# Kernel tuning notes

Measured on AMD Instinct MI355X. Metric: run time of the kernel, lower is better.

## Reference

```python
import jax, jax.numpy as jnp
import numpy as np

B, NX, W, DX, DY, D, H, P = 8, 512, 16, 1536, 1024, 768, 12, 8


def setup_inputs() -> dict:
    key = jax.random.key(0)
    ks = jax.random.split(key, 12)
    r = lambda k, s: jax.random.normal(k, s, dtype=jnp.float32) * 0.02
    return {
        "x": jax.random.normal(ks[0], (B, NX, DX), jnp.float32),
        "y": jax.random.normal(ks[1], (B, NX * W, DY), jnp.float32),
        "Wx": r(ks[2], (DX, D)), "bx": jnp.zeros((D,), jnp.float32),
        "Wy": r(ks[3], (DY, D)), "by": jnp.zeros((D,), jnp.float32),
        "prompt": r(ks[4], (1, P, D)),
        "Wq": r(ks[5], (D, D)), "bq": jnp.zeros((D,), jnp.float32),
        "Wk": r(ks[6], (D, D)), "bk": jnp.zeros((D,), jnp.float32),
        "Wv": r(ks[7], (D, D)), "bv": jnp.zeros((D,), jnp.float32),
        "Wo": r(ks[8], (D, D)), "bo": jnp.zeros((D,), jnp.float32),
        "ln_g": jnp.ones((D,), jnp.float32), "ln_b": jnp.zeros((D,), jnp.float32),
    }


def _l2n(f, eps=1e-6):
    return f / (jnp.linalg.norm(f, axis=-1, keepdims=True) + eps)


def reference(x, y, Wx, bx, Wy, by, prompt, Wq, bq, Wk, bk, Wv, bv, Wo, bo, ln_g, ln_b):
    dh = D // H
    scale = 1.0 / jnp.sqrt(jnp.float32(dh))
    xp = _l2n(x @ Wx + bx)            # [B,NX,D]
    yp = _l2n(y @ Wy + by)            # [B,NX*W,D]
    # In the original, only normalized_output[:,0:1] is kept per window, and
    # per-query attention is independent, so only query index 0 contributes.
    q = ((xp[:, 0] @ Wq) + bq).reshape(B, H, dh) * scale   # [B,H,dh]
    yw = yp.reshape(B, NX, W, D)                            # 16-token windows
    k = ((yw @ Wk) + bk).reshape(B, NX, W, H, dh)
    v = ((yw @ Wv) + bv).reshape(B, NX, W, H, dh)
    s = jnp.einsum('bhd,bnwhd->bhnw', q, k)                # [B,H,NX,W]
    a = jax.nn.softmax(s, axis=-1)
    ctx = jnp.einsum('bhnw,bnwhd->bnhd', a, v).reshape(B, NX, D)
    o = ctx @ Wo + bo                                      # attn out_proj
    mu = jnp.mean(o, axis=-1, keepdims=True)
    var = jnp.var(o, axis=-1, keepdims=True)
    normed = (o - mu) / jnp.sqrt(var + 1e-6) * ln_g + ln_b  # [B,NX,D]
    blocks = jnp.concatenate(
        [normed[:, :, None, :],
         jnp.broadcast_to(prompt[:, None], (B, NX, P, D))], axis=2)  # [B,NX,1+P,D]
    return blocks.reshape(B, NX * (1 + P), D)
```

## Files before the change

kernel.cpp:

```cpp
#include <hip/hip_runtime.h>
#include <stdint.h>

#define BQ 8
#define NXQ 512
#define WQ 16
#define DXQ 1536
#define DYQ 1024
#define DQ 768
#define HQ 12
#define PQ 8
#define MY 65536
#define BN_ROWS 4096

typedef __attribute__((ext_vector_type(8))) short short8;
typedef __attribute__((ext_vector_type(4))) float f32x4;
typedef unsigned short ushort_t;
typedef unsigned int uint_t;

__device__ __forceinline__ ushort_t f2bf(float f) {
  uint_t u = __float_as_uint(f);
  u += 0x7FFFu + ((u >> 16) & 1u);
  return (ushort_t)(u >> 16);
}
__device__ __forceinline__ float bf2f(ushort_t h) {
  return __uint_as_float(((uint_t)h) << 16);
}
__device__ __forceinline__ void gload_lds16(const void* g, void* l) {
  __builtin_amdgcn_global_load_lds(
      (__attribute__((address_space(1))) unsigned int*)(g),
      (__attribute__((address_space(3))) unsigned int*)(l), 16, 0, 0);
}

__global__ void k_conv(const float* __restrict__ y, const float* __restrict__ Wy,
                       const float* __restrict__ Wv, const float* __restrict__ Wo,
                       ushort_t* __restrict__ ybf, ushort_t* __restrict__ WyT,
                       ushort_t* __restrict__ WvT, ushort_t* __restrict__ WoT,
                       float* __restrict__ rowsq, float* __restrict__ oS12,
                       float* __restrict__ xw) {
  const int gstride = gridDim.x * blockDim.x;
  const int g0 = blockIdx.x * blockDim.x + threadIdx.x;
  const int NY8 = MY * DYQ / 8;
  for (int i = g0; i < NY8; i += gstride) {
    const float4* s = (const float4*)(y + (size_t)i * 8);
    float4 f0 = s[0], f1 = s[1];
    short8 hv;
    hv[0] = (short)f2bf(f0.x); hv[1] = (short)f2bf(f0.y);
    hv[2] = (short)f2bf(f0.z); hv[3] = (short)f2bf(f0.w);
    hv[4] = (short)f2bf(f1.x); hv[5] = (short)f2bf(f1.y);
    hv[6] = (short)f2bf(f1.z); hv[7] = (short)f2bf(f1.w);
    *(short8*)(ybf + (size_t)i * 8) = hv;
  }
  for (int i = g0; i < MY; i += gstride) rowsq[i] = 0.f;
  for (int i = g0; i < 2 * BN_ROWS; i += gstride) oS12[i] = 0.f;
  for (int i = g0; i < BQ * DQ; i += gstride) xw[i] = 0.f;
  const int N1 = DQ * DYQ;
  const int N2 = DQ * DQ;
  const int total = N1 + 2 * N2;
  for (int i = g0; i < total; i += gstride) {
    if (i < N1) {
      int n = i / DYQ, k = i - n * DYQ;
      WyT[i] = f2bf(Wy[k * DQ + n]);
    } else if (i < N1 + N2) {
      int j = i - N1;
      int n = j / DQ, k = j - n * DQ;
      WvT[j] = f2bf(Wv[k * DQ + n]);
    } else {
      int j = i - N1 - N2;
      int n = j / DQ, k = j - n * DQ;
      WoT[j] = f2bf(Wo[k * DQ + n]);
    }
  }
}

__global__ __launch_bounds__(128) void k_q1(const float* __restrict__ x,
                                            const float* __restrict__ Wx,
                                            const float* __restrict__ bx,
                                            float* __restrict__ xw) {
  const int b = blockIdx.x, c = blockIdx.y * 128 + threadIdx.x;
  const int kc = blockIdx.z;
  const float* xr = x + (size_t)b * NXQ * DXQ + kc * 192;
  const float* wp = Wx + (size_t)kc * 192 * DQ + c;
  float acc = (kc == 0) ? bx[c] : 0.f;
  for (int k = 0; k < 192; ++k) acc += xr[k] * wp[(size_t)k * DQ];
  atomicAdd(&xw[b * DQ + c], acc);
}

__global__ __launch_bounds__(128) void k_q2(const float* __restrict__ xw,
                                            const float* __restrict__ Wq,
                                            const float* __restrict__ bq,
                                            float* __restrict__ qv) {
  const int b = blockIdx.x, c = blockIdx.y * 128 + threadIdx.x;
  const float* xr = xw + b * DQ;
  float acc = 0.f, ss = 0.f;
  for (int k = 0; k < DQ; ++k) {
    float v = xr[k];
    acc += v * Wq[(size_t)k * DQ + c];
    ss += v * v;
  }
  const float inv = 1.0f / (sqrtf(ss) + 1e-6f);
  qv[b * DQ + c] = (acc * inv + bq[c]) * 0.125f;
}

__global__ void k_q3(const float* __restrict__ Wk, const float* __restrict__ bk,
                     const float* __restrict__ qv, float* __restrict__ qk,
                     float* __restrict__ cQ) {
  const int bh = blockIdx.x;
  const int b = bh / HQ, h = bh - b * HQ;
  const int tid = threadIdx.x;
  const float* q = qv + b * DQ + h * 64;
#pragma unroll
  for (int j = 0; j < 3; ++j) {
    int dd = tid + j * 256;
    float acc = 0.f;
    for (int j2 = 0; j2 < 64; ++j2) acc += Wk[(size_t)dd * DQ + h * 64 + j2] * q[j2];
    qk[(size_t)bh * DQ + dd] = acc;
  }
  if (tid == 0) {
    float acc = 0.f;
    for (int j2 = 0; j2 < 64; ++j2) acc += q[j2] * bk[h * 64 + j2];
    cQ[bh] = acc;
  }
}

#define YP_TSZ 49152
#define YP_NT 16
__global__ __launch_bounds__(512) void k_gemm_yp(const ushort_t* __restrict__ ybf,
                                                 const ushort_t* __restrict__ WyT,
                                                 const float* __restrict__ by,
                                                 ushort_t* __restrict__ z,
                                                 float* __restrict__ rowsqg) {
  __shared__ __align__(16) char smem[3 * YP_TSZ + 1024];
  float* rowsq_l = (float*)(smem + 3 * YP_TSZ);
  const int tid = threadIdx.x, lane = tid & 63, wv = tid >> 6;
  const int wvM = wv >> 2, wvN = wv & 3;
  const int g = blockIdx.x;
  const int m = (g / 48) * 8 + (g & 7);
  const int n = (g >> 3) % 6;
  const int mBase = m * 256, nBase = n * 128;
  if (tid < 256) rowsq_l[tid] = 0.f;

  const int l8 = lane >> 3;
  const int c8 = (lane & 7) ^ (l8 & 7);
  const ushort_t* aSrc[4]; const ushort_t* bSrc[2];
  int aDst[4], bDst[2];
#pragma unroll
  for (int j = 0; j < 4; ++j) {
    int r = wv * 32 + j * 8 + l8;
    aSrc[j] = ybf + (size_t)(mBase + r) * DYQ + c8 * 8;
    aDst[j] = (wv * 32 + j * 8) * 128;
  }
#pragma unroll
  for (int j = 0; j < 2; ++j) {
    int r = wv * 16 + j * 8 + l8;
    bSrc[j] = WyT + (size_t)(nBase + r) * DYQ + c8 * 8;
    bDst[j] = 32768 + (wv * 16 + j * 8) * 128;
  }
  const int q = lane >> 4;
  int aRowB[8], aSw[8], bRowB[2], bSw[2];
#pragma unroll
  for (int mf = 0; mf < 8; ++mf) {
    int r = wvM * 128 + mf * 16 + (lane & 15);
    aRowB[mf] = r * 128; aSw[mf] = r & 7;
  }
#pragma unroll
  for (int nf = 0; nf < 2; ++nf) {
    int r = wvN * 32 + nf * 16 + (lane & 15);
    bRowB[nf] = 32768 + r * 128; bSw[nf] = r & 7;
  }

#define YP_STAGE(dbuf, t)                                                      \
  {                                                                            \
    char* db = smem + (dbuf) * YP_TSZ;                                         \
    _Pragma("unroll") for (int j = 0; j < 4; ++j)                              \
        gload_lds16(aSrc[j] + (t) * 64, db + aDst[j]);                         \
    _Pragma("unroll") for (int j = 0; j < 2; ++j)                              \
        gload_lds16(bSrc[j] + (t) * 64, db + bDst[j]);                         \
  }

  f32x4 acc[8][2] = {};
  YP_STAGE(0, 0);
  YP_STAGE(1, 1);
  int bR = 0, bS = 2;
  for (int t = 0; t < YP_NT; ++t) {
    if (t < YP_NT - 1) {
      asm volatile("s_waitcnt vmcnt(6)" ::: "memory");
    } else {
      asm volatile("s_waitcnt vmcnt(0)" ::: "memory");
    }
    __builtin_amdgcn_s_barrier();
    __builtin_amdgcn_sched_barrier(0);
    if (t + 2 < YP_NT) YP_STAGE(bS, t + 2);
    const char* cur = smem + bR * YP_TSZ;
#pragma unroll
    for (int ks = 0; ks < 2; ++ks) {
      short8 af[8], bf[2];
#pragma unroll
      for (int mf = 0; mf < 8; ++mf)
        af[mf] = *(const short8*)(cur + aRowB[mf] + (((ks * 4 + q) ^ aSw[mf]) << 4));
#pragma unroll
      for (int nf = 0; nf < 2; ++nf)
        bf[nf] = *(const short8*)(cur + bRowB[nf] + (((ks * 4 + q) ^ bSw[nf]) << 4));
      __builtin_amdgcn_s_setprio(1);
#pragma unroll
      for (int nf = 0; nf < 2; ++nf)
#pragma unroll
        for (int mf = 0; mf < 8; ++mf)
          acc[mf][nf] = __builtin_amdgcn_mfma_f32_16x16x32_bf16(af[mf], bf[nf],
                                                                acc[mf][nf], 0, 0, 0);
      __builtin_amdgcn_s_setprio(0);
    }
    __builtin_amdgcn_sched_barrier(0);
    bR = (bR == 2) ? 0 : bR + 1;
    bS = (bS == 2) ? 0 : bS + 1;
  }
  __syncthreads();

  float byv[2];
#pragma unroll
  for (int nf = 0; nf < 2; ++nf) byv[nf] = by[nBase + wvN * 32 + nf * 16 + (lane & 15)];
#pragma unroll
  for (int mf = 0; mf < 8; ++mf) {
#pragma unroll
    for (int rr = 0; rr < 4; ++rr) {
      int row_l = wvM * 128 + mf * 16 + (lane >> 4) * 4 + rr;
      float ss = 0.f;
#pragma unroll
      for (int nf = 0; nf < 2; ++nf) {
        float zv = acc[mf][nf][rr] + byv[nf];
        ss += zv * zv;
        int col_l = wvN * 32 + nf * 16 + (lane & 15);
        *(ushort_t*)(smem + row_l * 256 + col_l * 2) = f2bf(zv);
      }
#pragma unroll
      for (int o = 1; o < 16; o <<= 1) ss += __shfl_xor(ss, o, 64);
      if ((lane & 15) == 0) atomicAdd(&rowsq_l[row_l], ss);
    }
  }
  __syncthreads();
  if (tid < 256) atomicAdd(&rowsqg[mBase + tid], rowsq_l[tid]);
#pragma unroll
  for (int it = 0; it < 8; ++it) {
    int row = it * 32 + (tid >> 4);
    int ch = tid & 15;
    uint4 v = *(const uint4*)(smem + row * 256 + ch * 16);
    *(uint4*)(z + (size_t)(mBase + row) * DQ + nBase + ch * 8) = v;
  }
}

__global__ __launch_bounds__(256) void k_attn(const ushort_t* __restrict__ z,
                                              const float* __restrict__ rowsqg,
                                              const float* __restrict__ qk,
                                              const float* __restrict__ cQ,
                                              ushort_t* __restrict__ p) {
  __shared__ __align__(16) char smem[16 * 1552 + 192 * 4 * 2 + 64];
  float* s_l = (float*)(smem + 16 * 1552);
  float* a_l = s_l + 192;
  float* inv_l = a_l + 192;
  const int bn = blockIdx.x, b = bn >> 9;
  const int tid = threadIdx.x;
  if (tid < 16) inv_l[tid] = 1.0f / (sqrtf(rowsqg[bn * 16 + tid]) + 1e-6f);
  for (int j = tid; j < 16 * 96; j += 256) {
    int w = j / 96, ch = j - w * 96;
    *(short8*)(smem + w * 1552 + ch * 16) =
        *(const short8*)(z + ((size_t)bn * 16 + w) * DQ + ch * 8);
  }
  __syncthreads();
  if (tid < 192) {
    int h = tid >> 4, w = tid & 15;
    const float4* qkp = (const float4*)(qk + (size_t)(b * HQ + h) * DQ);
    float acc = 0.f;
    const char* yrow = smem + w * 1552;
    for (int dc = 0; dc < 192; ++dc) {
      float4 q4 = qkp[dc];
      uint2 hh = *(const uint2*)(yrow + dc * 8);
      acc += q4.x * bf2f((ushort_t)(hh.x & 0xffff));
      acc += q4.y * bf2f((ushort_t)(hh.x >> 16));
      acc += q4.z * bf2f((ushort_t)(hh.y & 0xffff));
      acc += q4.w * bf2f((ushort_t)(hh.y >> 16));
    }
    s_l[tid] = acc * inv_l[w] + cQ[b * HQ + h];
  }
  __syncthreads();
  if (tid < 12) {
    float mx = -1e30f;
#pragma unroll
    for (int w = 0; w < 16; ++w) mx = fmaxf(mx, s_l[tid * 16 + w]);
    float sm = 0.f, ev[16];
#pragma unroll
    for (int w = 0; w < 16; ++w) {
      ev[w] = __expf(s_l[tid * 16 + w] - mx);
      sm += ev[w];
    }
    float rden = 1.0f / sm;
#pragma unroll
    for (int w = 0; w < 16; ++w) a_l[tid * 16 + w] = ev[w] * rden * inv_l[w];
  }
  __syncthreads();
  float zr[16][3];
#pragma unroll
  for (int w = 0; w < 16; ++w)
#pragma unroll
    for (int i = 0; i < 3; ++i)
      zr[w][i] = bf2f(*(const ushort_t*)(smem + w * 1552 + (tid + i * 256) * 2));
  for (int h = 0; h < HQ; ++h) {
    float acc0 = 0.f, acc1 = 0.f, acc2 = 0.f;
#pragma unroll
    for (int w = 0; w < 16; ++w) {
      float aw = a_l[h * 16 + w];
      acc0 += aw * zr[w][0];
      acc1 += aw * zr[w][1];
      acc2 += aw * zr[w][2];
    }
    size_t base = ((size_t)bn * HQ + h) * DQ + tid;
    p[base] = f2bf(acc0);
    p[base + 256] = f2bf(acc1);
    p[base + 512] = f2bf(acc2);
  }
}

#define PV_TSZ 24576
__global__ __launch_bounds__(256) void k_gemm_pv(const ushort_t* __restrict__ p,
                                                 const ushort_t* __restrict__ WvT,
                                                 const float* __restrict__ bv,
                                                 ushort_t* __restrict__ ctx) {
  __shared__ __align__(16) char smem[3 * PV_TSZ];
  const int tid = threadIdx.x, lane = tid & 63, wv = tid >> 6;
  const int wvM = wv >> 1, wvN = wv & 1;
  const int mBase = blockIdx.x * 128, h = blockIdx.y;
  const int l8 = lane >> 3;
  const int c8 = (lane & 7) ^ (l8 & 7);
  const ushort_t* aSrc[4]; const ushort_t* bSrc[2];
  int aDst[4], bDst[2];
#pragma unroll
  for (int j = 0; j < 4; ++j) {
    int r = wv * 32 + j * 8 + l8;
    aSrc[j] = p + ((size_t)(mBase + r) * HQ + h) * DQ + c8 * 8;
    aDst[j] = (wv * 32 + j * 8) * 128;
  }
#pragma unroll
  for (int j = 0; j < 2; ++j) {
    int r = wv * 16 + j * 8 + l8;
    bSrc[j] = WvT + (size_t)(h * 64 + r) * DQ + c8 * 8;
    bDst[j] = 16384 + (wv * 16 + j * 8) * 128;
  }
  const int q = lane >> 4;
  int aRowB[4], aSw[4], bRowB[2], bSw[2];
#pragma unroll
  for (int mf = 0; mf < 4; ++mf) {
    int r = wvM * 64 + mf * 16 + (lane & 15);
    aRowB[mf] = r * 128; aSw[mf] = r & 7;
  }
#pragma unroll
  for (int nf = 0; nf < 2; ++nf) {
    int r = wvN * 32 + nf * 16 + (lane & 15);
    bRowB[nf] = 16384 + r * 128; bSw[nf] = r & 7;
  }
#define PV_STAGE(dbuf, t)                                                      \
  {                                                                            \
    char* db = smem + (dbuf) * PV_TSZ;                                         \
    _Pragma("unroll") for (int j = 0; j < 4; ++j)                              \
        gload_lds16(aSrc[j] + (t) * 64, db + aDst[j]);                         \
    _Pragma("unroll") for (int j = 0; j < 2; ++j)                              \
        gload_lds16(bSrc[j] + (t) * 64, db + bDst[j]);                         \
  }
  f32x4 acc[4][2] = {};
  PV_STAGE(0, 0);
  PV_STAGE(1, 1);
  int bR = 0, bS = 2;
  for (int t = 0; t < 12; ++t) {
    if (t < 11) {
      asm volatile("s_waitcnt vmcnt(6)" ::: "memory");
    } else {
      asm volatile("s_waitcnt vmcnt(0)" ::: "memory");
    }
    __builtin_amdgcn_s_barrier();
    __builtin_amdgcn_sched_barrier(0);
    if (t + 2 < 12) PV_STAGE(bS, t + 2);
    const char* cur = smem + bR * PV_TSZ;
#pragma unroll
    for (int ks = 0; ks < 2; ++ks) {
      short8 af[4], bf[2];
#pragma unroll
      for (int mf = 0; mf < 4; ++mf)
        af[mf] = *(const short8*)(cur + aRowB[mf] + (((ks * 4 + q) ^ aSw[mf]) << 4));
#pragma unroll
      for (int nf = 0; nf < 2; ++nf)
        bf[nf] = *(const short8*)(cur + bRowB[nf] + (((ks * 4 + q) ^ bSw[nf]) << 4));
      __builtin_amdgcn_s_setprio(1);
#pragma unroll
      for (int nf = 0; nf < 2; ++nf)
#pragma unroll
        for (int mf = 0; mf < 4; ++mf)
          acc[mf][nf] = __builtin_amdgcn_mfma_f32_16x16x32_bf16(af[mf], bf[nf],
                                                                acc[mf][nf], 0, 0, 0);
      __builtin_amdgcn_s_setprio(0);
    }
    __builtin_amdgcn_sched_barrier(0);
    bR = (bR == 2) ? 0 : bR + 1;
    bS = (bS == 2) ? 0 : bS + 1;
  }
#pragma unroll
  for (int nf = 0; nf < 2; ++nf) {
    int col = h * 64 + wvN * 32 + nf * 16 + (lane & 15);
    float bvv = bv[col];
#pragma unroll
    for (int mf = 0; mf < 4; ++mf)
#pragma unroll
      for (int rr = 0; rr < 4; ++rr) {
        int row = mBase + wvM * 64 + mf * 16 + (lane >> 4) * 4 + rr;
        ctx[(size_t)row * DQ + col] = f2bf(acc[mf][nf][rr] + bvv);
      }
  }
}

__global__ __launch_bounds__(256) void k_gemm_o(const ushort_t* __restrict__ ctx,
                                                const ushort_t* __restrict__ WoT,
                                                const float* __restrict__ bo,
                                                float* __restrict__ o,
                                                float* __restrict__ oS12) {
  __shared__ __align__(16) char smem[3 * PV_TSZ];
  const int tid = threadIdx.x, lane = tid & 63, wv = tid >> 6;
  const int wvM = wv >> 1, wvN = wv & 1;
  const int mBase = blockIdx.x * 128, nBase = blockIdx.y * 64;
  const int l8 = lane >> 3;
  const int c8 = (lane & 7) ^ (l8 & 7);
  const ushort_t* aSrc[4]; const ushort_t* bSrc[2];
  int aDst[4], bDst[2];
#pragma unroll
  for (int j = 0; j < 4; ++j) {
    int r = wv * 32 + j * 8 + l8;
    aSrc[j] = ctx + (size_t)(mBase + r) * DQ + c8 * 8;
    aDst[j] = (wv * 32 + j * 8) * 128;
  }
#pragma unroll
  for (int j = 0; j < 2; ++j) {
    int r = wv * 16 + j * 8 + l8;
    bSrc[j] = WoT + (size_t)(nBase + r) * DQ + c8 * 8;
    bDst[j] = 16384 + (wv * 16 + j * 8) * 128;
  }
  const int q = lane >> 4;
  int aRowB[4], aSw[4], bRowB[2], bSw[2];
#pragma unroll
  for (int mf = 0; mf < 4; ++mf) {
    int r = wvM * 64 + mf * 16 + (lane & 15);
    aRowB[mf] = r * 128; aSw[mf] = r & 7;
  }
#pragma unroll
  for (int nf = 0; nf < 2; ++nf) {
    int r = wvN * 32 + nf * 16 + (lane & 15);
    bRowB[nf] = 16384 + r * 128; bSw[nf] = r & 7;
  }
  f32x4 acc[4][2] = {};
#define O_STAGE(dbuf, t)                                                       \
  {                                                                            \
    char* db = smem + (dbuf) * PV_TSZ;                                         \
    _Pragma("unroll") for (int j = 0; j < 4; ++j)                              \
        gload_lds16(aSrc[j] + (t) * 64, db + aDst[j]);                         \
    _Pragma("unroll") for (int j = 0; j < 2; ++j)                              \
        gload_lds16(bSrc[j] + (t) * 64, db + bDst[j]);                         \
  }
  O_STAGE(0, 0);
  O_STAGE(1, 1);
  int bR = 0, bS = 2;
  for (int t = 0; t < 12; ++t) {
    if (t < 11) {
      asm volatile("s_waitcnt vmcnt(6)" ::: "memory");
    } else {
      asm volatile("s_waitcnt vmcnt(0)" ::: "memory");
    }
    __builtin_amdgcn_s_barrier();
    __builtin_amdgcn_sched_barrier(0);
    if (t + 2 < 12) O_STAGE(bS, t + 2);
    const char* cur = smem + bR * PV_TSZ;
#pragma unroll
    for (int ks = 0; ks < 2; ++ks) {
      short8 af[4], bf[2];
#pragma unroll
      for (int mf = 0; mf < 4; ++mf)
        af[mf] = *(const short8*)(cur + aRowB[mf] + (((ks * 4 + q) ^ aSw[mf]) << 4));
#pragma unroll
      for (int nf = 0; nf < 2; ++nf)
        bf[nf] = *(const short8*)(cur + bRowB[nf] + (((ks * 4 + q) ^ bSw[nf]) << 4));
      __builtin_amdgcn_s_setprio(1);
#pragma unroll
      for (int nf = 0; nf < 2; ++nf)
#pragma unroll
        for (int mf = 0; mf < 4; ++mf)
          acc[mf][nf] = __builtin_amdgcn_mfma_f32_16x16x32_bf16(af[mf], bf[nf],
                                                                acc[mf][nf], 0, 0, 0);
      __builtin_amdgcn_s_setprio(0);
    }
    __builtin_amdgcn_sched_barrier(0);
    bR = (bR == 2) ? 0 : bR + 1;
    bS = (bS == 2) ? 0 : bS + 1;
  }
  float bo0 = bo[nBase + wvN * 32 + (lane & 15)];
  float bo1 = bo[nBase + wvN * 32 + 16 + (lane & 15)];
#pragma unroll
  for (int mf = 0; mf < 4; ++mf)
#pragma unroll
    for (int rr = 0; rr < 4; ++rr) {
      int row = mBase + wvM * 64 + mf * 16 + (lane >> 4) * 4 + rr;
      float z0 = acc[mf][0][rr] + bo0;
      float z1 = acc[mf][1][rr] + bo1;
      o[(size_t)row * DQ + nBase + wvN * 32 + (lane & 15)] = z0;
      o[(size_t)row * DQ + nBase + wvN * 32 + 16 + (lane & 15)] = z1;
      float s1 = z0 + z1, s2 = z0 * z0 + z1 * z1;
#pragma unroll
      for (int ofs = 1; ofs < 16; ofs <<= 1) {
        s1 += __shfl_xor(s1, ofs, 64);
        s2 += __shfl_xor(s2, ofs, 64);
      }
      if ((lane & 15) == 0) {
        atomicAdd(&oS12[row], s1);
        atomicAdd(&oS12[BN_ROWS + row], s2);
      }
    }
}

__global__ __launch_bounds__(256) void k_out(const float* __restrict__ o,
                                             const float* __restrict__ oS12,
                                             const float* __restrict__ ln_g,
                                             const float* __restrict__ ln_b,
                                             const float* __restrict__ prompt,
                                             float* __restrict__ out) {
  const int row = blockIdx.x;
  const int tid = threadIdx.x;
  float mu = oS12[row] * (1.0f / DQ);
  float va = oS12[BN_ROWS + row] * (1.0f / DQ) - mu * mu;
  float rstd = rsqrtf(va + 1e-6f);
  int b = row >> 9, n = row & 511;
  size_t obase = ((size_t)b * (NXQ * (PQ + 1)) + (size_t)n * (PQ + 1)) * DQ;
#pragma unroll
  for (int j = 0; j < 3; ++j) {
    int col = tid + j * 256;
    out[obase + col] = (o[(size_t)row * DQ + col] - mu) * rstd * ln_g[col] + ln_b[col];
  }
#pragma unroll
  for (int pi = 0; pi < PQ; ++pi)
#pragma unroll
    for (int j = 0; j < 3; ++j) {
      int col = tid + j * 256;
      out[obase + (size_t)(1 + pi) * DQ + col] = prompt[pi * DQ + col];
    }
}

extern "C" void kernel_launch(void* const* d_in, const int* in_sizes, int n_in,
                              void* d_out, int out_size, void* d_ws, size_t ws_size,
                              hipStream_t stream) {
  (void)in_sizes; (void)n_in; (void)out_size; (void)ws_size;
  const float* x    = (const float*)d_in[0];
  const float* y    = (const float*)d_in[1];
  const float* Wx   = (const float*)d_in[2];
  const float* bx   = (const float*)d_in[3];
  const float* Wy   = (const float*)d_in[4];
  const float* by   = (const float*)d_in[5];
  const float* prom = (const float*)d_in[6];
  const float* Wq   = (const float*)d_in[7];
  const float* bq   = (const float*)d_in[8];
  const float* Wk   = (const float*)d_in[9];
  const float* bk   = (const float*)d_in[10];
  const float* Wv   = (const float*)d_in[11];
  const float* bv   = (const float*)d_in[12];
  const float* Wo   = (const float*)d_in[13];
  const float* bo   = (const float*)d_in[14];
  const float* lng  = (const float*)d_in[15];
  const float* lnb  = (const float*)d_in[16];
  float* out = (float*)d_out;
  char* ws = (char*)d_ws;

  size_t oWyT = 0;
  size_t oWvT = oWyT + (size_t)DQ * DYQ * 2;
  size_t oWoT = oWvT + (size_t)DQ * DQ * 2;
  size_t oXw  = oWoT + (size_t)DQ * DQ * 2;
  size_t oQ   = oXw + (size_t)BQ * DQ * 4 + 256;
  size_t oQK  = oQ + (size_t)BQ * DQ * 4;
  size_t oC   = oQK + (size_t)BQ * HQ * DQ * 4;
  size_t oRq  = oC + 1024;
  size_t oS   = oRq + (size_t)MY * 4;
  size_t oYbf = oS + (size_t)2 * BN_ROWS * 4;
  size_t oZ   = oYbf + (size_t)MY * DYQ * 2;
  size_t oP   = oYbf;
  size_t oCtx = oYbf + (size_t)BN_ROWS * HQ * DQ * 2;
  size_t oO   = oZ;

  ushort_t* WyT = (ushort_t*)(ws + oWyT);
  ushort_t* WvT = (ushort_t*)(ws + oWvT);
  ushort_t* WoT = (ushort_t*)(ws + oWoT);
  float* xw  = (float*)(ws + oXw);
  float* qv  = (float*)(ws + oQ);
  float* qk  = (float*)(ws + oQK);
  float* cQ  = (float*)(ws + oC);
  float* rowsq = (float*)(ws + oRq);
  float* oS12  = (float*)(ws + oS);
  ushort_t* ybf  = (ushort_t*)(ws + oYbf);
  ushort_t* zbuf = (ushort_t*)(ws + oZ);
  ushort_t* p    = (ushort_t*)(ws + oP);
  ushort_t* ctx  = (ushort_t*)(ws + oCtx);
  float* obuf    = (float*)(ws + oO);

  k_conv<<<dim3(4096), dim3(256), 0, stream>>>(y, Wy, Wv, Wo, ybf, WyT, WvT, WoT,
                                               rowsq, oS12, xw);
  k_q1<<<dim3(BQ, 6, 8), dim3(128), 0, stream>>>(x, Wx, bx, xw);
  k_q2<<<dim3(BQ, 6), dim3(128), 0, stream>>>(xw, Wq, bq, qv);
  k_q3<<<dim3(BQ * HQ), dim3(256), 0, stream>>>(Wk, bk, qv, qk, cQ);
  k_gemm_yp<<<dim3(1536), dim3(512), 0, stream>>>(ybf, WyT, by, zbuf, rowsq);
  k_attn<<<dim3(BN_ROWS), dim3(256), 0, stream>>>(zbuf, rowsq, qk, cQ, p);
  k_gemm_pv<<<dim3(BN_ROWS / 128, HQ), dim3(256), 0, stream>>>(p, WvT, bv, ctx);
  k_gemm_o<<<dim3(BN_ROWS / 128, DQ / 64), dim3(256), 0, stream>>>(ctx, WoT, bo, obuf, oS12);
  k_out<<<dim3(BN_ROWS), dim3(256), 0, stream>>>(obuf, oS12, lng, lnb, prom, out);
}
```

Measured before the change: 471.4 us.

## Enlarge yp GEMM tile to 256x256 with split-K double-buffered LDS staging

The y-projection GEMM now computes 256x256 output tiles per block instead of 256x128, which halves the grid and doubles the reuse of each loaded A tile. Staging changes from a three-deep ring of 64-wide K tiles to a two-buffer scheme, with each buffer split into two 32-wide halves that are prefetched one half-step ahead and use a new swizzle. The pv and o GEMMs lose their setprio and sched_barrier hints. In exchange, accumulator register pressure doubles with one block per CU, and the waits and barriers per K-tile become finer-grained.

```diff
diff --git a/kernel.cpp b/kernel.cpp
--- a/kernel.cpp
+++ b/kernel.cpp
@@ -122,102 +122,95 @@
   }
 }
 
-#define YP_TSZ 49152
-#define YP_NT 16
-__global__ __launch_bounds__(512) void k_gemm_yp(const ushort_t* __restrict__ ybf,
-                                                 const ushort_t* __restrict__ WyT,
-                                                 const float* __restrict__ by,
-                                                 ushort_t* __restrict__ z,
-                                                 float* __restrict__ rowsqg) {
-  __shared__ __align__(16) char smem[3 * YP_TSZ + 1024];
-  float* rowsq_l = (float*)(smem + 3 * YP_TSZ);
+__global__ __launch_bounds__(512, 1) void k_gemm_yp(const ushort_t* __restrict__ ybf,
+                                                    const ushort_t* __restrict__ WyT,
+                                                    const float* __restrict__ by,
+                                                    ushort_t* __restrict__ z,
+                                                    float* __restrict__ rowsqg) {
+  __shared__ __align__(16) char smem[131072 + 1024];
+  float* rowsq_l = (float*)(smem + 131072);
   const int tid = threadIdx.x, lane = tid & 63, wv = tid >> 6;
   const int wvM = wv >> 2, wvN = wv & 3;
   const int g = blockIdx.x;
-  const int m = (g / 48) * 8 + (g & 7);
-  const int n = (g >> 3) % 6;
-  const int mBase = m * 256, nBase = n * 128;
+  const int m = (g / 24) * 8 + (g & 7);
+  const int n = (g >> 3) % 3;
+  const int mBase = m * 256, nBase = n * 256;
   if (tid < 256) rowsq_l[tid] = 0.f;
 
-  const int l8 = lane >> 3;
-  const int c8 = (lane & 7) ^ (l8 & 7);
-  const ushort_t* aSrc[4]; const ushort_t* bSrc[2];
-  int aDst[4], bDst[2];
-#pragma unroll
-  for (int j = 0; j < 4; ++j) {
-    int r = wv * 32 + j * 8 + l8;
-    aSrc[j] = ybf + (size_t)(mBase + r) * DYQ + c8 * 8;
-    aDst[j] = (wv * 32 + j * 8) * 128;
-  }
+  const int sr = lane >> 2;
+  const int sc = (lane & 3) ^ (sr & 3);
+  const ushort_t* aQ[2]; const ushort_t* bQ[2];
+  int qDst[2];
 #pragma unroll
   for (int j = 0; j < 2; ++j) {
-    int r = wv * 16 + j * 8 + l8;
-    bSrc[j] = WyT + (size_t)(nBase + r) * DYQ + c8 * 8;
-    bDst[j] = 32768 + (wv * 16 + j * 8) * 128;
+    int r = wv * 32 + j * 16 + sr;
+    aQ[j] = ybf + (size_t)(mBase + r) * DYQ + sc * 8;
+    bQ[j] = WyT + (size_t)(nBase + r) * DYQ + sc * 8;
+    qDst[j] = (wv * 32 + j * 16) * 64;
   }
   const int q = lane >> 4;
-  int aRowB[8], aSw[8], bRowB[2], bSw[2];
+  int aFr[8], bFr[4];
 #pragma unroll
   for (int mf = 0; mf < 8; ++mf) {
     int r = wvM * 128 + mf * 16 + (lane & 15);
-    aRowB[mf] = r * 128; aSw[mf] = r & 7;
-  }
-#pragma unroll
-  for (int nf = 0; nf < 2; ++nf) {
-    int r = wvN * 32 + nf * 16 + (lane & 15);
-    bRowB[nf] = 32768 + r * 128; bSw[nf] = r & 7;
-  }
-
-#define YP_STAGE(dbuf, t)                                                      \
+    aFr[mf] = r * 64 + ((q ^ (r & 3)) << 4);
+  }
+#pragma unroll
+  for (int nf = 0; nf < 4; ++nf) {
+    int r = wvN * 64 + nf * 16 + (lane & 15);
+    bFr[nf] = 32768 + r * 64 + ((q ^ (r & 3)) << 4);
+  }
+
+#define YP_STAGE(bufb, tt, ks)                                                 \
   {                                                                            \
-    char* db = smem + (dbuf) * YP_TSZ;                                         \
-    _Pragma("unroll") for (int j = 0; j < 4; ++j)                              \
-        gload_lds16(aSrc[j] + (t) * 64, db + aDst[j]);                         \
+    char* db = smem + (bufb) * 65536 + (ks) * 16384;                           \
     _Pragma("unroll") for (int j = 0; j < 2; ++j)                              \
-        gload_lds16(bSrc[j] + (t) * 64, db + bDst[j]);                         \
-  }
-
-  f32x4 acc[8][2] = {};
-  YP_STAGE(0, 0);
-  YP_STAGE(1, 1);
-  int bR = 0, bS = 2;
-  for (int t = 0; t < YP_NT; ++t) {
-    if (t < YP_NT - 1) {
-      asm volatile("s_waitcnt vmcnt(6)" ::: "memory");
-    } else {
-      asm volatile("s_waitcnt vmcnt(0)" ::: "memory");
-    }
-    __builtin_amdgcn_s_barrier();
-    __builtin_amdgcn_sched_barrier(0);
-    if (t + 2 < YP_NT) YP_STAGE(bS, t + 2);
-    const char* cur = smem + bR * YP_TSZ;
+        gload_lds16(aQ[j] + (tt) * 64 + (ks) * 32, db + qDst[j]);              \
+    _Pragma("unroll") for (int j = 0; j < 2; ++j)                              \
+        gload_lds16(bQ[j] + (tt) * 64 + (ks) * 32, db + 32768 + qDst[j]);      \
+  }
+
+  f32x4 acc[8][4] = {};
+  YP_STAGE(0, 0, 0);
+  YP_STAGE(0, 0, 1);
+  for (int t = 0; t < 16; ++t) {
+    const int c = t & 1;
+    const char* cb = smem + c * 65536;
 #pragma unroll
     for (int ks = 0; ks < 2; ++ks) {
-      short8 af[8], bf[2];
+      if (t == 15 && ks == 1) {
+        asm volatile("s_waitcnt vmcnt(0)" ::: "memory");
+      } else {
+        asm volatile("s_waitcnt vmcnt(4)" ::: "memory");
+      }
+      __builtin_amdgcn_s_barrier();
+      __builtin_amdgcn_sched_barrier(0);
+      short8 af[8], bf[4];
 #pragma unroll
       for (int mf = 0; mf < 8; ++mf)
-        af[mf] = *(const short8*)(cur + aRowB[mf] + (((ks * 4 + q) ^ aSw[mf]) << 4));
-#pragma unroll
-      for (int nf = 0; nf < 2; ++nf)
-        bf[nf] = *(const short8*)(cur + bRowB[nf] + (((ks * 4 + q) ^ bSw[nf]) << 4));
+        af[mf] = *(const short8*)(cb + ks * 16384 + aFr[mf]);
+#pragma unroll
+      for (int nf = 0; nf < 4; ++nf)
+        bf[nf] = *(const short8*)(cb + ks * 16384 + bFr[nf]);
+      if (t < 15) YP_STAGE(c ^ 1, t + 1, ks);
+      asm volatile("s_waitcnt lgkmcnt(0)" ::: "memory");
+      __builtin_amdgcn_sched_barrier(0);
       __builtin_amdgcn_s_setprio(1);
 #pragma unroll
-      for (int nf = 0; nf < 2; ++nf)
+      for (int nf = 0; nf < 4; ++nf)
 #pragma unroll
         for (int mf = 0; mf < 8; ++mf)
           acc[mf][nf] = __builtin_amdgcn_mfma_f32_16x16x32_bf16(af[mf], bf[nf],
                                                                 acc[mf][nf], 0, 0, 0);
       __builtin_amdgcn_s_setprio(0);
-    }
-    __builtin_amdgcn_sched_barrier(0);
-    bR = (bR == 2) ? 0 : bR + 1;
-    bS = (bS == 2) ? 0 : bS + 1;
+      __builtin_amdgcn_sched_barrier(0);
+    }
   }
   __syncthreads();
 
-  float byv[2];
-#pragma unroll
-  for (int nf = 0; nf < 2; ++nf) byv[nf] = by[nBase + wvN * 32 + nf * 16 + (lane & 15)];
+  float byv[4];
+#pragma unroll
+  for (int nf = 0; nf < 4; ++nf) byv[nf] = by[nBase + wvN * 64 + nf * 16 + (lane & 15)];
 #pragma unroll
   for (int mf = 0; mf < 8; ++mf) {
 #pragma unroll
@@ -225,11 +218,11 @@
       int row_l = wvM * 128 + mf * 16 + (lane >> 4) * 4 + rr;
       float ss = 0.f;
 #pragma unroll
-      for (int nf = 0; nf < 2; ++nf) {
+      for (int nf = 0; nf < 4; ++nf) {
         float zv = acc[mf][nf][rr] + byv[nf];
         ss += zv * zv;
-        int col_l = wvN * 32 + nf * 16 + (lane & 15);
-        *(ushort_t*)(smem + row_l * 256 + col_l * 2) = f2bf(zv);
+        int col_l = wvN * 64 + nf * 16 + (lane & 15);
+        *(ushort_t*)(smem + row_l * 512 + col_l * 2) = f2bf(zv);
       }
 #pragma unroll
       for (int o = 1; o < 16; o <<= 1) ss += __shfl_xor(ss, o, 64);
@@ -239,10 +232,10 @@
   __syncthreads();
   if (tid < 256) atomicAdd(&rowsqg[mBase + tid], rowsq_l[tid]);
 #pragma unroll
-  for (int it = 0; it < 8; ++it) {
-    int row = it * 32 + (tid >> 4);
-    int ch = tid & 15;
-    uint4 v = *(const uint4*)(smem + row * 256 + ch * 16);
+  for (int it = 0; it < 16; ++it) {
+    int row = it * 16 + (tid >> 5);
+    int ch = tid & 31;
+    uint4 v = *(const uint4*)(smem + row * 512 + ch * 16);
     *(uint4*)(z + (size_t)(mBase + row) * DQ + nBase + ch * 8) = v;
   }
 }
@@ -386,16 +379,13 @@
 #pragma unroll
       for (int nf = 0; nf < 2; ++nf)
         bf[nf] = *(const short8*)(cur + bRowB[nf] + (((ks * 4 + q) ^ bSw[nf]) << 4));
-      __builtin_amdgcn_s_setprio(1);
 #pragma unroll
       for (int nf = 0; nf < 2; ++nf)
 #pragma unroll
         for (int mf = 0; mf < 4; ++mf)
           acc[mf][nf] = __builtin_amdgcn_mfma_f32_16x16x32_bf16(af[mf], bf[nf],
                                                                 acc[mf][nf], 0, 0, 0);
-      __builtin_amdgcn_s_setprio(0);
-    }
-    __builtin_amdgcn_sched_barrier(0);
+    }
     bR = (bR == 2) ? 0 : bR + 1;
     bS = (bS == 2) ? 0 : bS + 1;
   }
@@ -481,16 +471,13 @@
 #pragma unroll
       for (int nf = 0; nf < 2; ++nf)
         bf[nf] = *(const short8*)(cur + bRowB[nf] + (((ks * 4 + q) ^ bSw[nf]) << 4));
-      __builtin_amdgcn_s_setprio(1);
 #pragma unroll
       for (int nf = 0; nf < 2; ++nf)
 #pragma unroll
         for (int mf = 0; mf < 4; ++mf)
           acc[mf][nf] = __builtin_amdgcn_mfma_f32_16x16x32_bf16(af[mf], bf[nf],
                                                                 acc[mf][nf], 0, 0, 0);
-      __builtin_amdgcn_s_setprio(0);
-    }
-    __builtin_amdgcn_sched_barrier(0);
+    }
     bR = (bR == 2) ? 0 : bR + 1;
     bS = (bS == 2) ? 0 : bS + 1;
   }
@@ -604,7 +591,7 @@
   k_q1<<<dim3(BQ, 6, 8), dim3(128), 0, stream>>>(x, Wx, bx, xw);
   k_q2<<<dim3(BQ, 6), dim3(128), 0, stream>>>(xw, Wq, bq, qv);
   k_q3<<<dim3(BQ * HQ), dim3(256), 0, stream>>>(Wk, bk, qv, qk, cQ);
-  k_gemm_yp<<<dim3(1536), dim3(512), 0, stream>>>(ybf, WyT, by, zbuf, rowsq);
+  k_gemm_yp<<<dim3(768), dim3(512), 0, stream>>>(ybf, WyT, by, zbuf, rowsq);
   k_attn<<<dim3(BN_ROWS), dim3(256), 0, stream>>>(zbuf, rowsq, qk, cQ, p);
   k_gemm_pv<<<dim3(BN_ROWS / 128, HQ), dim3(256), 0, stream>>>(p, WvT, bv, ctx);
   k_gemm_o<<<dim3(BN_ROWS / 128, DQ / 64), dim3(256), 0, stream>>>(ctx, WoT, bo, obuf, oS12);
```

New measurement: 450.7 us. 4.4% less time.
